# Kernel tuning notes

Measured on AMD Instinct MI355X. Metric: run time of the kernel, lower is better.

The kernel has to match this reference:

```python
import jax, jax.numpy as jnp
import numpy as np

LAM_CONSIST = 0.1
LAM_LR = 1.0
LAM_PAIR = 1.0


def _cubic(x, a=-0.75):
    # PyTorch bicubic kernel (a = -0.75)
    ax = jnp.abs(x)
    ax2 = ax * ax
    ax3 = ax2 * ax
    f1 = (a + 2.0) * ax3 - (a + 3.0) * ax2 + 1.0
    f2 = a * ax3 - 5.0 * a * ax2 + 8.0 * a * ax - 4.0 * a
    return jnp.where(ax <= 1.0, f1, jnp.where(ax < 2.0, f2, 0.0))


def _resize_matrix(in_size: int, out_size: int) -> jnp.ndarray:
    """Weight matrix [out_size, in_size] for antialiased bicubic resize
    (align_corners=False, antialias=True, border replicate) as in
    F.interpolate(..., mode='bicubic', antialias=True)."""
    scale = in_size / out_size
    s_aa = max(scale, 1.0)  # widen kernel when downscaling (antialias)
    support = 2.0 * s_aa
    ext = int(np.ceil(support)) + 1
    centers = (np.arange(out_size, dtype=np.float64) + 0.5) * scale - 0.5
    idx = np.arange(-ext, in_size + ext)
    dist = (idx[None, :] - centers[:, None]) / s_aa  # [out, in+2ext]
    w = _cubic(jnp.asarray(dist, dtype=jnp.float32))
    w = w / jnp.sum(w, axis=1, keepdims=True)  # torch normalizes window weights
    idx_c = np.clip(idx, 0, in_size - 1)  # clamp -> replicate border
    M = jnp.zeros((out_size, in_size), dtype=jnp.float32).at[:, idx_c].add(w)
    return M


def _resize_bicubic_aa(img: jnp.ndarray, th: int, tw: int) -> jnp.ndarray:
    # img: [B, C, H, W] -> [B, C, th, tw], separable resize via two matmuls
    _, _, h, w = img.shape
    Mh = _resize_matrix(h, th)  # [th, h]
    Mw = _resize_matrix(w, tw)  # [tw, w]
    return jnp.einsum('oh,bchw,pw->bcop', Mh, img, Mw)


def setup_inputs() -> dict:
    key = jax.random.key(0)
    k1, k2, k3 = jax.random.split(key, 3)
    pred_hr = jax.random.normal(k1, (32, 3, 512, 512), dtype=jnp.float32)
    target_hr = jax.random.normal(k2, (32, 3, 512, 512), dtype=jnp.float32)
    lr_ref = jax.random.normal(k3, (32, 3, 128, 128), dtype=jnp.float32)
    scale = jnp.full((32,), 4.0, dtype=jnp.float32)  # uniform -> static sizes
    return {"pred_hr": pred_hr, "target_hr": target_hr, "lr_ref": lr_ref, "scale": scale}


def reference(pred_hr, target_hr, lr_ref, scale):
    pix = jnp.mean(jnp.abs(pred_hr - target_hr))
    # project_scale(pred_hr, src=scale, dst=1): uniform scale=4 ->
    # target size == lr_ref spatial size (static, read from lr_ref shape)
    th, tw = lr_ref.shape[-2], lr_ref.shape[-1]
    pred_lr = _resize_bicubic_aa(pred_hr, th, tw)
    lr_term = jnp.mean(jnp.abs(pred_lr - lr_ref))
    pair_term = jnp.float32(0.0)  # pair_pred_hr / pair_scale are None
    consist = LAM_LR * lr_term + LAM_PAIR * pair_term
    total = pix + LAM_CONSIST * consist
    return (total, pix, consist, lr_term, pair_term)
```

## Files before the change

### kernel.cpp

```cpp
#include <hip/hip_runtime.h>

#define HW    512
#define OUTW  128
#define NIMG  96
#define N_HR  ((long long)NIMG*HW*HW)
#define N_LR  ((long long)NIMG*OUTW*OUTW)
#define NBLK  (NIMG*8)

__device__ __forceinline__ float cubic075(float x){
    float ax = fabsf(x);
    float ax2 = ax*ax, ax3 = ax2*ax;
    const float A = -0.75f;
    float f1 = (A+2.f)*ax3 - (A+3.f)*ax2 + 1.f;
    float f2 = A*ax3 - 5.f*A*ax2 + 8.f*A*ax - 4.f*A;
    return ax <= 1.f ? f1 : (ax < 2.f ? f2 : 0.f);
}

__device__ __forceinline__ void get_weights(float w[16]){
    float s = 0.f;
#pragma unroll
    for (int k = 0; k < 16; ++k){
        float d = ((float)k - 7.5f) * 0.25f;
        w[k] = cubic075(d);
        s += w[k];
    }
#pragma unroll
    for (int k = 0; k < 16; ++k) w[k] /= s;
}

__global__ __launch_bounds__(256, 3) void kmain(const float* __restrict__ pred,
                                                const float* __restrict__ tgt,
                                                const float* __restrict__ lr,
                                                double* __restrict__ part1,
                                                double* __restrict__ part2){
    const int b   = blockIdx.x;
    const int W   = ((b & 7) * (NBLK/8)) + (b >> 3);
    const int img = W >> 3;
    const int grp = W & 7;
    const int o0  = grp << 4;
    const int s   = (o0 << 2) - 6;
    const int tid = threadIdx.x;
    const int w   = tid >> 6;
    const int l   = tid & 63;

    __shared__ float  ring[32][128];
    __shared__ double sred[8];

    float wt[16]; get_weights(wt);
    const float* P = pred + (size_t)img * (HW*HW);
    const float* T = tgt  + (size_t)img * (HW*HW);
    const float* L = lr   + (size_t)img * (OUTW*OUTW);

    float pix_acc = 0.f, lr_acc = 0.f;

    int r0 = min(HW-1, max(0, s + w));
    int r1 = min(HW-1, max(0, s + 4 + w));
    const float4* rp0 = (const float4*)(P + (size_t)r0 * HW);
    const float4* rp1 = (const float4*)(P + (size_t)r1 * HW);
    float4 c0 = rp0[2*l], c1 = rp0[2*l+1];
    float4 n0 = rp1[2*l], n1 = rp1[2*l+1];
    float4 tc0, tc1, tn0, tn1;
    if (w >= 2){
        const float4* tp = (const float4*)(T + (size_t)(s + 4 + w) * HW);
        tn0 = tp[2*l]; tn1 = tp[2*l+1];
    }

    for (int i = 0; i < 19; ++i){
        const int jcur = 4*i + w;
        const int j2   = jcur + 8;
        float4 f0, f1, tf0, tf1;
        if (i < 17){
            int rn = min(HW-1, max(0, s + j2));
            const float4* rp = (const float4*)(P + (size_t)rn * HW);
            f0 = rp[2*l]; f1 = rp[2*l+1];
        }
        if (j2 < 70){
            const float4* tp = (const float4*)(T + (size_t)(s + j2) * HW);
            tf0 = tp[2*l]; tf1 = tp[2*l+1];
        }

        const float p0=c0.x,p1v=c0.y,p2v=c0.z,p3=c0.w,
                    p4=c1.x,p5=c1.y,p6=c1.z,p7=c1.w;

        if (jcur >= 6 && jcur < 70){
            pix_acc += fabsf(p0-tc0.x)+fabsf(p1v-tc0.y)+fabsf(p2v-tc0.z)+fabsf(p3-tc0.w)
                     + fabsf(p4-tc1.x)+fabsf(p5-tc1.y)+fabsf(p6-tc1.z)+fabsf(p7-tc1.w);
        }

        float Lm6 = __shfl_up(p2v,1,64), Lm5 = __shfl_up(p3,1,64),
              Lm4 = __shfl_up(p4,1,64),  Lm3 = __shfl_up(p5,1,64),
              Lm2 = __shfl_up(p6,1,64),  Lm1 = __shfl_up(p7,1,64);
        float R8  = __shfl_down(p0,1,64), R9  = __shfl_down(p1v,1,64),
              R10 = __shfl_down(p2v,1,64),R11 = __shfl_down(p3,1,64),
              R12 = __shfl_down(p4,1,64), R13 = __shfl_down(p5,1,64);
        if (l == 0){ Lm6=p0; Lm5=p0; Lm4=p0; Lm3=p0; Lm2=p0; Lm1=p0; }
        if (l == 63){ R8=p7; R9=p7; R10=p7; R11=p7; R12=p7; R13=p7; }

        float w20[20] = {Lm6,Lm5,Lm4,Lm3,Lm2,Lm1,p0,p1v,p2v,p3,p4,p5,p6,p7,
                         R8,R9,R10,R11,R12,R13};
        float h0 = 0.f, h1 = 0.f;
#pragma unroll
        for (int k = 0; k < 16; ++k){
            h0 += wt[k]*w20[k];
            h1 += wt[k]*w20[k+4];
        }
        float2 st; st.x = h0; st.y = h1;
        *(float2*)&ring[jcur & 31][2*l] = st;

        __syncthreads();

        if (i >= 3 && tid < 128){
            const int q = i - 3;
            float acc = 0.f;
#pragma unroll
            for (int r = 0; r < 16; ++r)
                acc += wt[r] * ring[(4*q + r) & 31][tid];
            lr_acc += fabsf(acc - L[(size_t)(o0 + q) * OUTW + tid]);
        }

        c0=n0; c1=n1; n0=f0; n1=f1;
        tc0=tn0; tc1=tn1; tn0=tf0; tn1=tf1;
    }

#pragma unroll
    for (int off = 32; off > 0; off >>= 1){
        pix_acc += __shfl_down(pix_acc, off, 64);
        lr_acc  += __shfl_down(lr_acc,  off, 64);
    }
    if (l == 0){ sred[w] = (double)pix_acc; sred[4+w] = (double)lr_acc; }
    __syncthreads();
    if (tid == 0)  part1[b] = sred[0]+sred[1]+sred[2]+sred[3];
    if (tid == 64) part2[b] = sred[4]+sred[5]+sred[6]+sred[7];
}

__global__ __launch_bounds__(256) void k3(const double* __restrict__ part1,
                                          const double* __restrict__ part2,
                                          float* __restrict__ out){
    const int t = threadIdx.x;
    double v1 = 0.0, v2 = 0.0;
    for (int i = t; i < NBLK; i += 256){
        v1 += part1[i];
        v2 += part2[i];
    }
#pragma unroll
    for (int off = 32; off > 0; off >>= 1){
        v1 += __shfl_down(v1, off, 64);
        v2 += __shfl_down(v2, off, 64);
    }
    __shared__ double s1[4], s2[4];
    const int lane = t & 63, wid = t >> 6;
    if (lane == 0){ s1[wid] = v1; s2[wid] = v2; }
    __syncthreads();
    if (t == 0){
        double S1 = s1[0]+s1[1]+s1[2]+s1[3];
        double S2 = s2[0]+s2[1]+s2[2]+s2[3];
        float pix     = (float)(S1 / (double)N_HR);
        float lr_term = (float)(S2 / (double)N_LR);
        float pair    = 0.f;
        float consist = 1.0f * lr_term + 1.0f * pair;
        float total   = pix + 0.1f * consist;
        out[0] = total; out[1] = pix; out[2] = consist; out[3] = lr_term; out[4] = pair;
    }
}

extern "C" void kernel_launch(void* const* d_in, const int* in_sizes, int n_in,
                              void* d_out, int out_size, void* d_ws, size_t ws_size,
                              hipStream_t stream){
    const float* pred = (const float*)d_in[0];
    const float* tgt  = (const float*)d_in[1];
    const float* lrr  = (const float*)d_in[2];
    float* out = (float*)d_out;

    double* part1 = (double*)d_ws;
    double* part2 = part1 + NBLK;

    kmain<<<NBLK, 256, 0, stream>>>(pred, tgt, lrr, part1, part2);
    k3<<<1, 256, 0, stream>>>(part1, part2, out);
}
```

Before: 233.0 us.

## Restructure resize kernel: 512 threads, one output column per thread, full-tile smem

Doubles the block to 512 threads and gives each thread one output column, which it computes from five overlapping float4 loads instead of wave shuffles. The horizontal pass now writes every row into a full 76x128 shared buffer, leaving one barrier in place of a per-row ring buffer with a sync on every iteration. The vertical pass then runs on all threads at once. This removes the per-iteration synchronisation and shuffle overhead, but gives up register prefetch pipelining and reads overlapping global data redundantly, which relies on the cache.

```diff
diff --git a/kernel.cpp b/kernel.cpp
--- a/kernel.cpp
+++ b/kernel.cpp
@@ -28,7 +28,7 @@
     for (int k = 0; k < 16; ++k) w[k] /= s;
 }
 
-__global__ __launch_bounds__(256, 3) void kmain(const float* __restrict__ pred,
+__global__ __launch_bounds__(512, 6) void kmain(const float* __restrict__ pred,
                                                 const float* __restrict__ tgt,
                                                 const float* __restrict__ lr,
                                                 double* __restrict__ part1,
@@ -40,97 +40,99 @@
     const int o0  = grp << 4;
     const int s   = (o0 << 2) - 6;
     const int tid = threadIdx.x;
-    const int w   = tid >> 6;
-    const int l   = tid & 63;
+    const int rg  = tid >> 7;
+    const int o   = tid & 127;
 
-    __shared__ float  ring[32][128];
-    __shared__ double sred[8];
+    __shared__ float  hbuf[76][128];
+    __shared__ double sred[16];
 
     float wt[16]; get_weights(wt);
     const float* P = pred + (size_t)img * (HW*HW);
     const float* T = tgt  + (size_t)img * (HW*HW);
     const float* L = lr   + (size_t)img * (OUTW*OUTW);
 
+    int bq[5];
+#pragma unroll
+    for (int k = 0; k < 5; ++k)
+        bq[k] = min(508, max(0, 4*o - 8 + 4*k));
+    const int ctr = 4*o;
+
     float pix_acc = 0.f, lr_acc = 0.f;
 
-    int r0 = min(HW-1, max(0, s + w));
-    int r1 = min(HW-1, max(0, s + 4 + w));
-    const float4* rp0 = (const float4*)(P + (size_t)r0 * HW);
-    const float4* rp1 = (const float4*)(P + (size_t)r1 * HW);
-    float4 c0 = rp0[2*l], c1 = rp0[2*l+1];
-    float4 n0 = rp1[2*l], n1 = rp1[2*l+1];
-    float4 tc0, tc1, tn0, tn1;
-    if (w >= 2){
-        const float4* tp = (const float4*)(T + (size_t)(s + 4 + w) * HW);
-        tn0 = tp[2*l]; tn1 = tp[2*l+1];
+    for (int i = 0; i < 19; ++i){
+        const int j   = 4*i + rg;
+        const int hin = min(HW-1, max(0, s + j));
+        const float* R  = P + (size_t)hin * HW;
+        const float* TR = T + (size_t)hin * HW;
+
+        float4 q0 = *(const float4*)(R + bq[0]);
+        float4 q1 = *(const float4*)(R + bq[1]);
+        float4 q2 = *(const float4*)(R + bq[2]);
+        float4 q3 = *(const float4*)(R + bq[3]);
+        float4 q4 = *(const float4*)(R + bq[4]);
+        float4 tq = *(const float4*)(TR + ctr);
+
+        float t0=q0.z, t1=q0.w, t2=q1.x, t3=q1.y, t4=q1.z, t5=q1.w,
+              t6=q2.x, t7=q2.y, t8=q2.z, t9=q2.w, t10=q3.x, t11=q3.y,
+              t12=q3.z, t13=q3.w, t14=q4.x, t15=q4.y;
+        const int c0 = 4*o - 6;
+        t0  = (c0 +  0 <   0) ? q0.x : t0;
+        t1  = (c0 +  1 <   0) ? q0.x : t1;
+        t2  = (c0 +  2 <   0) ? q0.x : t2;
+        t3  = (c0 +  3 <   0) ? q0.x : t3;
+        t4  = (c0 +  4 <   0) ? q0.x : t4;
+        t5  = (c0 +  5 <   0) ? q0.x : t5;
+        t10 = (c0 + 10 > 511) ? q4.w : t10;
+        t11 = (c0 + 11 > 511) ? q4.w : t11;
+        t12 = (c0 + 12 > 511) ? q4.w : t12;
+        t13 = (c0 + 13 > 511) ? q4.w : t13;
+        t14 = (c0 + 14 > 511) ? q4.w : t14;
+        t15 = (c0 + 15 > 511) ? q4.w : t15;
+
+        float h = wt[0]*t0 + wt[1]*t1 + wt[2]*t2 + wt[3]*t3
+                + wt[4]*t4 + wt[5]*t5 + wt[6]*t6 + wt[7]*t7
+                + wt[8]*t8 + wt[9]*t9 + wt[10]*t10 + wt[11]*t11
+                + wt[12]*t12 + wt[13]*t13 + wt[14]*t14 + wt[15]*t15;
+        hbuf[j][o] = h;
+
+        if (j >= 6 && j < 70){
+            pix_acc += fabsf(q2.x-tq.x) + fabsf(q2.y-tq.y)
+                     + fabsf(q2.z-tq.z) + fabsf(q2.w-tq.w);
+        }
     }
 
-    for (int i = 0; i < 19; ++i){
-        const int jcur = 4*i + w;
-        const int j2   = jcur + 8;
-        float4 f0, f1, tf0, tf1;
-        if (i < 17){
-            int rn = min(HW-1, max(0, s + j2));
-            const float4* rp = (const float4*)(P + (size_t)rn * HW);
-            f0 = rp[2*l]; f1 = rp[2*l+1];
-        }
-        if (j2 < 70){
-            const float4* tp = (const float4*)(T + (size_t)(s + j2) * HW);
-            tf0 = tp[2*l]; tf1 = tp[2*l+1];
-        }
+    __syncthreads();
 
-        const float p0=c0.x,p1v=c0.y,p2v=c0.z,p3=c0.w,
-                    p4=c1.x,p5=c1.y,p6=c1.z,p7=c1.w;
-
-        if (jcur >= 6 && jcur < 70){
-            pix_acc += fabsf(p0-tc0.x)+fabsf(p1v-tc0.y)+fabsf(p2v-tc0.z)+fabsf(p3-tc0.w)
-                     + fabsf(p4-tc1.x)+fabsf(p5-tc1.y)+fabsf(p6-tc1.z)+fabsf(p7-tc1.w);
-        }
-
-        float Lm6 = __shfl_up(p2v,1,64), Lm5 = __shfl_up(p3,1,64),
-              Lm4 = __shfl_up(p4,1,64),  Lm3 = __shfl_up(p5,1,64),
-              Lm2 = __shfl_up(p6,1,64),  Lm1 = __shfl_up(p7,1,64);
-        float R8  = __shfl_down(p0,1,64), R9  = __shfl_down(p1v,1,64),
-              R10 = __shfl_down(p2v,1,64),R11 = __shfl_down(p3,1,64),
-              R12 = __shfl_down(p4,1,64), R13 = __shfl_down(p5,1,64);
-        if (l == 0){ Lm6=p0; Lm5=p0; Lm4=p0; Lm3=p0; Lm2=p0; Lm1=p0; }
-        if (l == 63){ R8=p7; R9=p7; R10=p7; R11=p7; R12=p7; R13=p7; }
-
-        float w20[20] = {Lm6,Lm5,Lm4,Lm3,Lm2,Lm1,p0,p1v,p2v,p3,p4,p5,p6,p7,
-                         R8,R9,R10,R11,R12,R13};
-        float h0 = 0.f, h1 = 0.f;
 #pragma unroll
-        for (int k = 0; k < 16; ++k){
-            h0 += wt[k]*w20[k];
-            h1 += wt[k]*w20[k+4];
-        }
-        float2 st; st.x = h0; st.y = h1;
-        *(float2*)&ring[jcur & 31][2*l] = st;
-
-        __syncthreads();
-
-        if (i >= 3 && tid < 128){
-            const int q = i - 3;
-            float acc = 0.f;
+    for (int m = 0; m < 4; ++m){
+        const int q = rg + 4*m;
+        float acc = 0.f;
 #pragma unroll
-            for (int r = 0; r < 16; ++r)
-                acc += wt[r] * ring[(4*q + r) & 31][tid];
-            lr_acc += fabsf(acc - L[(size_t)(o0 + q) * OUTW + tid]);
-        }
-
-        c0=n0; c1=n1; n0=f0; n1=f1;
-        tc0=tn0; tc1=tn1; tn0=tf0; tn1=tf1;
+        for (int r = 0; r < 16; ++r)
+            acc += wt[r] * hbuf[4*q + r][o];
+        lr_acc += fabsf(acc - L[(size_t)(o0 + q) * OUTW + o]);
     }
 
+    const int l = tid & 63, wv = tid >> 6;
 #pragma unroll
     for (int off = 32; off > 0; off >>= 1){
         pix_acc += __shfl_down(pix_acc, off, 64);
         lr_acc  += __shfl_down(lr_acc,  off, 64);
     }
-    if (l == 0){ sred[w] = (double)pix_acc; sred[4+w] = (double)lr_acc; }
+    if (l == 0){ sred[wv] = (double)pix_acc; sred[8+wv] = (double)lr_acc; }
     __syncthreads();
-    if (tid == 0)  part1[b] = sred[0]+sred[1]+sred[2]+sred[3];
-    if (tid == 64) part2[b] = sred[4]+sred[5]+sred[6]+sred[7];
+    if (tid == 0){
+        double S1 = 0.0;
+#pragma unroll
+        for (int k = 0; k < 8; ++k) S1 += sred[k];
+        part1[b] = S1;
+    }
+    if (tid == 64){
+        double S2 = 0.0;
+#pragma unroll
+        for (int k = 0; k < 8; ++k) S2 += sred[8+k];
+        part2[b] = S2;
+    }
 }
 
 __global__ __launch_bounds__(256) void k3(const double* __restrict__ part1,
@@ -174,6 +176,6 @@
     double* part1 = (double*)d_ws;
     double* part2 = part1 + NBLK;
 
-    kmain<<<NBLK, 256, 0, stream>>>(pred, tgt, lrr, part1, part2);
+    kmain<<<NBLK, 512, 0, stream>>>(pred, tgt, lrr, part1, part2);
     k3<<<1, 256, 0, stream>>>(part1, part2, out);
 }
```

Result: no change. 234.0 us (+0.4%).
